# Kernel tuning notes

Measured on AMD Instinct MI355X. Metric: run time of the kernel, lower is better.

Reference implementation:

```python
import jax, jax.numpy as jnp
import numpy as np

B, C, IMG, P = 32, 3, 224, 16
D, H, L, F, NCLS = 768, 12, 12, 3072, 1000
NP = (IMG // P) ** 2  # 196
DH = D // H  # 64
EPS = 1e-5


def _ln(x, g, b):
    m = jnp.mean(x, axis=-1, keepdims=True)
    v = jnp.mean(jnp.square(x - m), axis=-1, keepdims=True)
    return (x - m) * jax.lax.rsqrt(v + EPS) * g + b


def setup_inputs() -> dict:
    key = jax.random.key(0)
    ks = iter(jax.random.split(key, 32))
    s = 0.02
    rn = lambda shape: jax.random.normal(next(ks), shape, dtype=jnp.float32) * s
    inp = {
        "x": jax.random.normal(next(ks), (B, C, IMG, IMG), dtype=jnp.float32),
        "Wp": rn((P * P * C, D)), "bp": jnp.zeros((D,), jnp.float32),
        "cls": rn((1, 1, D)), "pos": rn((1, NP + 1, D)),
        # per-layer stacked params (leading dim L)
        "ln1_g": jnp.ones((L, D), jnp.float32), "ln1_b": jnp.zeros((L, D), jnp.float32),
        "Wq": rn((L, H, D, DH)), "bq": jnp.zeros((L, H, DH), jnp.float32),
        "Wk": rn((L, H, D, DH)), "bk": jnp.zeros((L, H, DH), jnp.float32),
        "Wv": rn((L, H, D, DH)), "bv": jnp.zeros((L, H, DH), jnp.float32),
        "Wo": rn((L, D, D)), "bo": jnp.zeros((L, D), jnp.float32),
        "ln2_g": jnp.ones((L, D), jnp.float32), "ln2_b": jnp.zeros((L, D), jnp.float32),
        "W1": rn((L, D, F)), "b1": jnp.zeros((L, F), jnp.float32),
        "W2": rn((L, F, D)), "b2": jnp.zeros((L, D), jnp.float32),
        # classification head
        "hln_g": jnp.ones((D,), jnp.float32), "hln_b": jnp.zeros((D,), jnp.float32),
        "hW1": rn((D, D)), "hb1": jnp.zeros((D,), jnp.float32),
        "hW2": rn((D, NCLS)), "hb2": jnp.zeros((NCLS,), jnp.float32),
    }
    return inp


def _vit(x, Wp, bp, cls, pos, ln1_g, ln1_b, Wq, bq, Wk, bk, Wv, bv, Wo, bo,
         ln2_g, ln2_b, W1, b1, W2, b2, hln_g, hln_b, hW1, hb1, hW2, hb2):
    b = x.shape[0]
    g = IMG // P
    # nn.Unfold(k=16, s=16): channel order (c, kh, kw), patch order (ph, pw)
    patches = x.reshape(b, C, g, P, g, P).transpose(0, 2, 4, 1, 3, 5).reshape(b, NP, C * P * P)
    h = patches @ Wp + bp  # [b, NP, D]
    h = jnp.concatenate([jnp.broadcast_to(cls, (b, 1, D)), h], axis=1) + pos  # [b, S, D]

    scale = 1.0 / jnp.sqrt(jnp.asarray(DH, h.dtype))

    def step(h, p):
        g1, b1_, wq, bq_, wk, bk_, wv, bv_, wo, bo_, g2, b2_, w1, bb1, w2, bb2 = p
        xn = _ln(h, g1, b1_)
        q = jnp.einsum('bsd,hde->bhse', xn, wq) + bq_[:, None, :]
        k = jnp.einsum('bsd,hde->bhse', xn, wk) + bk_[:, None, :]
        v = jnp.einsum('bsd,hde->bhse', xn, wv) + bv_[:, None, :]
        scores = jnp.einsum('bhse,bhte->bhst', q, k) * scale
        attn = jax.nn.softmax(scores, axis=-1)
        o = jnp.einsum('bhst,bhte->bhse', attn, v)  # [b,H,S,DH]
        o = o.transpose(0, 2, 1, 3).reshape(b, -1, D)  # concat heads
        h = o @ wo + bo_ + h
        xn = _ln(h, g2, b2_)
        h = jax.nn.gelu(xn @ w1 + bb1, approximate=False) @ w2 + bb2 + h
        return h, None

    params = (ln1_g, ln1_b, Wq, bq, Wk, bk, Wv, bv, Wo, bo, ln2_g, ln2_b, W1, b1, W2, b2)
    h, _ = jax.lax.scan(step, h, params)

    c = h[:, 0, :]
    c = _ln(c, hln_g, hln_b)
    return jax.nn.gelu(c @ hW1 + hb1, approximate=False) @ hW2 + hb2


def reference(x, Wp, bp, cls, pos, ln1_g, ln1_b, Wq, bq, Wk, bk, Wv, bv, Wo, bo,
              ln2_g, ln2_b, W1, b1, W2, b2, hln_g, hln_b, hW1, hb1, hW2, hb2):
    return _vit(x, Wp, bp, cls, pos, ln1_g, ln1_b, Wq, bq, Wk, bk, Wv, bv, Wo, bo,
                ln2_g, ln2_b, W1, b1, W2, b2, hln_g, hln_b, hW1, hb1, hW2, hb2)
```

## Files before the change

### kernel.cpp

```cpp
#include <hip/hip_runtime.h>

typedef unsigned short u16;
typedef __attribute__((ext_vector_type(8))) short short8;
typedef __attribute__((ext_vector_type(4))) float f32x4;

#define NTOK 6304
#define SP 197

#define OFF_WQKVT 0L
#define OFF_WOT   42467328L
#define OFF_W1T   56623104L
#define OFF_W2T   113246208L
#define OFF_WPT   169869312L
#define OFF_BQKV  171048960L
#define OFF_H     171159552L
#define OFF_XN    190525440L
#define OFF_QKV   200208384L
#define OFF_SC    229257216L
#define OFF_PM1   288867840L
#define OFF_VT    327599616L
#define OFF_CN    340182528L
#define OFF_T1    340280832L
#define WS_NEEDED 340379136L

__device__ __forceinline__ u16 f2bf(float x) {
  unsigned int u = __float_as_uint(x);
  u += 0x7fffu + ((u >> 16) & 1u);
  return (u16)(u >> 16);
}

__device__ __forceinline__ float gelu_f(float x) {
  return 0.5f * x * (1.0f + erff(x * 0.70710678118654752f));
}

__device__ __forceinline__ void gload_lds16(const void* g, void* l) {
  __builtin_amdgcn_global_load_lds(
      (const __attribute__((address_space(1))) unsigned int*)g,
      (__attribute__((address_space(3))) unsigned int*)l, 16, 0, 0);
}

__device__ __forceinline__ void stage_tile(const u16* src, int ld,
                                           int row0, int maxrow, int k0,
                                           char* ldsbase, int t) {
  const int wbase = t & 192;
#pragma unroll
  for (int p = 0; p < 4; ++p) {
    int idx = p * 256 + t;
    int r = idx >> 3;
    int cl = idx & 7;
    int cg = cl ^ (r & 7);
    int rr = row0 + r;
    rr = rr > maxrow ? maxrow : rr;
    const u16* g = src + (long)rr * ld + (k0 + cg * 8);
    char* lp = ldsbase + (long)(p * 256 + wbase) * 16;
    gload_lds16(g, lp);
  }
}

template <bool BIAS, bool GELU, bool RES, bool OBF16, bool REMAP>
__global__ __launch_bounds__(256, 3) void gemm_k(
    const u16* __restrict__ A, int lda,
    const u16* __restrict__ Bm, int ldb,
    void* Cv, int ldc,
    const float* __restrict__ bias, const float* res, int ldres,
    int M, int N, int K, int tilesN) {
  __shared__ float4 smemv[2048];
  char* smem = (char*)smemv;

  const int t = threadIdx.x;
  const int nwg = gridDim.x;
  const int orig = blockIdx.x;
  const int q8 = nwg >> 3, r8 = nwg & 7;
  const int xcd = orig & 7, loc = orig >> 3;
  const int wg =
      (xcd < r8 ? xcd * (q8 + 1) : r8 * (q8 + 1) + (xcd - r8) * q8) + loc;
  const int tn = wg % tilesN, tm = wg / tilesN;
  const int m0 = tm * 128, n0 = tn * 128;
  const int l = t & 63;
  const int lr = l & 15, kb = l >> 4;
  const int wr = (t >> 7) & 1, wc = (t >> 6) & 1;

  const f32x4 zf = {0.f, 0.f, 0.f, 0.f};
  f32x4 acc[4][4];
#pragma unroll
  for (int m = 0; m < 4; ++m)
#pragma unroll
    for (int n = 0; n < 4; ++n) acc[m][n] = zf;

  const int KT = K >> 6;
  for (int kt = 0; kt < KT; ++kt) {
    stage_tile(A, lda, m0, M - 1, kt * 64, smem, t);
    stage_tile(Bm, ldb, n0, N - 1, kt * 64, smem + 16384, t);
    __syncthreads();
    const char* Ab = smem;
    const char* Bb = smem + 16384;
#pragma unroll
    for (int kk = 0; kk < 2; ++kk) {
      const int cla = ((kk << 2) + kb) ^ (lr & 7);
      short8 af[4], bfv[4];
#pragma unroll
      for (int m = 0; m < 4; ++m)
        af[m] = *(const short8*)(Ab + ((wr * 64 + m * 16 + lr) * 128 + cla * 16));
#pragma unroll
      for (int n = 0; n < 4; ++n)
        bfv[n] = *(const short8*)(Bb + ((wc * 64 + n * 16 + lr) * 128 + cla * 16));
#pragma unroll
      for (int m = 0; m < 4; ++m)
#pragma unroll
        for (int n = 0; n < 4; ++n)
          acc[m][n] = __builtin_amdgcn_mfma_f32_16x16x32_bf16(af[m], bfv[n],
                                                              acc[m][n], 0, 0, 0);
    }
    __syncthreads();
  }

#pragma unroll
  for (int n = 0; n < 4; ++n) {
    const int gc = n0 + wc * 64 + n * 16 + lr;
    if (gc >= N) continue;
    const float bv = BIAS ? bias[gc] : 0.0f;
#pragma unroll
    for (int m = 0; m < 4; ++m) {
#pragma unroll
      for (int j = 0; j < 4; ++j) {
        const int gr = m0 + wr * 64 + m * 16 + kb * 4 + j;
        if (gr >= M) continue;
        float v = acc[m][n][j] + bv;
        if (RES) v += res[(long)gr * ldres + gc];
        if (GELU) v = gelu_f(v);
        long orow = gr;
        if (REMAP) orow = (long)(gr / 196) * 197 + (gr % 196) + 1;
        if (OBF16)
          ((u16*)Cv)[orow * (long)ldc + gc] = f2bf(v);
        else
          ((float*)Cv)[orow * (long)ldc + gc] = v;
      }
    }
  }
}

__global__ __launch_bounds__(256) void k_attn(const u16* __restrict__ qkv,
                                              u16* __restrict__ o) {
  __shared__ __align__(16) u16 Kb[208 * 72];
  __shared__ __align__(16) u16 Vt[64 * 232];
  __shared__ __align__(16) u16 Pl[4][16 * 232];

  const int t = threadIdx.x;
  const int z = blockIdx.x;
  const int b = z / 12, hh = z % 12;
  const long qbase = (long)b * SP * 2304 + hh * 64;

#pragma unroll
  for (int p = 0; p < 7; ++p) {
    int idx = p * 256 + t;
    int row = idx >> 3, c = idx & 7;
    short8 kv = {0, 0, 0, 0, 0, 0, 0, 0};
    short8 vv = {0, 0, 0, 0, 0, 0, 0, 0};
    if (row < SP) {
      kv = *(const short8*)(qkv + qbase + 768 + (long)row * 2304 + c * 8);
      vv = *(const short8*)(qkv + qbase + 1536 + (long)row * 2304 + c * 8);
    }
    if (row < 208) *(short8*)(&Kb[row * 72 + c * 8]) = kv;
#pragma unroll
    for (int j = 0; j < 8; ++j) Vt[(c * 8 + j) * 232 + row] = ((const u16*)&vv)[j];
  }
  __syncthreads();

  const int l = t & 63, wid = t >> 6;
  const int lr = l & 15, kb = l >> 4;
  u16* Pw = Pl[wid];
  const f32x4 zf = {0.f, 0.f, 0.f, 0.f};

  for (int st = wid; st < 13; st += 4) {
    int qrow = st * 16 + lr;
    qrow = qrow > SP - 1 ? SP - 1 : qrow;
    short8 qf[2];
#pragma unroll
    for (int kk = 0; kk < 2; ++kk)
      qf[kk] = *(const short8*)(qkv + qbase + (long)qrow * 2304 + kk * 32 + kb * 8);

    f32x4 s[13];
#pragma unroll
    for (int nt = 0; nt < 13; ++nt) {
      s[nt] = zf;
#pragma unroll
      for (int kk = 0; kk < 2; ++kk) {
        short8 kf = *(const short8*)(&Kb[(nt * 16 + lr) * 72 + kk * 32 + kb * 8]);
        s[nt] = __builtin_amdgcn_mfma_f32_16x16x32_bf16(qf[kk], kf, s[nt], 0, 0, 0);
      }
    }

    float mx[4] = {-1e30f, -1e30f, -1e30f, -1e30f};
#pragma unroll
    for (int nt = 0; nt < 13; ++nt) {
      const bool pred = (nt < 12) | (lr < 5);
#pragma unroll
      for (int j = 0; j < 4; ++j) {
        float v = s[nt][j] * 0.125f;
        s[nt][j] = v;
        if (pred) mx[j] = fmaxf(mx[j], v);
      }
    }
#pragma unroll
    for (int o4 = 1; o4 < 16; o4 <<= 1)
#pragma unroll
      for (int j = 0; j < 4; ++j) mx[j] = fmaxf(mx[j], __shfl_xor(mx[j], o4));
    float sum[4] = {0.f, 0.f, 0.f, 0.f};
#pragma unroll
    for (int nt = 0; nt < 13; ++nt) {
      const bool pred = (nt < 12) | (lr < 5);
#pragma unroll
      for (int j = 0; j < 4; ++j) {
        float p = pred ? __expf(s[nt][j] - mx[j]) : 0.f;
        s[nt][j] = p;
        sum[j] += p;
      }
    }
#pragma unroll
    for (int o4 = 1; o4 < 16; o4 <<= 1)
#pragma unroll
      for (int j = 0; j < 4; ++j) sum[j] += __shfl_xor(sum[j], o4);
    float inv[4];
#pragma unroll
    for (int j = 0; j < 4; ++j) inv[j] = 1.0f / sum[j];

#pragma unroll
    for (int nt = 0; nt < 13; ++nt)
#pragma unroll
      for (int j = 0; j < 4; ++j)
        Pw[(kb * 4 + j) * 232 + nt * 16 + lr] = f2bf(s[nt][j] * inv[j]);
#pragma unroll
    for (int j = 0; j < 4; ++j) Pw[(kb * 4 + j) * 232 + 208 + lr] = 0;

    short8 pf[7];
#pragma unroll
    for (int kk = 0; kk < 7; ++kk)
      pf[kk] = *(const short8*)(&Pw[lr * 232 + kk * 32 + kb * 8]);
#pragma unroll
    for (int dt = 0; dt < 4; ++dt) {
      f32x4 oacc = zf;
#pragma unroll
      for (int kk = 0; kk < 7; ++kk) {
        short8 vf = *(const short8*)(&Vt[(dt * 16 + lr) * 232 + kk * 32 + kb * 8]);
        oacc = __builtin_amdgcn_mfma_f32_16x16x32_bf16(pf[kk], vf, oacc, 0, 0, 0);
      }
#pragma unroll
      for (int j = 0; j < 4; ++j) {
        int qr = st * 16 + kb * 4 + j;
        if (qr < SP)
          o[((long)b * SP + qr) * 768 + hh * 64 + dt * 16 + lr] = f2bf(oacc[j]);
      }
    }
  }
}

__global__ void k_wt64(const float* __restrict__ W, u16* __restrict__ out,
                       int sel) {
  __shared__ float tile[32][33];
  const int z = blockIdx.z;
  const int ly = z / 12, hh = z % 12;
  const float* ip = W + (long)z * 768 * 64;
  u16* op = out + (long)ly * 2304 * 768 + ((long)sel * 768 + hh * 64) * 768;
  const int c0 = blockIdx.x * 32, r0 = blockIdx.y * 32;
  const int tx = threadIdx.x, ty = threadIdx.y;
#pragma unroll
  for (int i = 0; i < 4; ++i)
    tile[ty + i * 8][tx] = ip[(long)(r0 + ty + i * 8) * 64 + c0 + tx];
  __syncthreads();
#pragma unroll
  for (int i = 0; i < 4; ++i)
    op[(long)(c0 + ty + i * 8) * 768 + r0 + tx] = f2bf(tile[tx][ty + i * 8]);
}

__global__ void k_bqkv(const float* __restrict__ bq, const float* __restrict__ bk,
                       const float* __restrict__ bv, float* __restrict__ out) {
  int idx = blockIdx.x * 256 + threadIdx.x;
  if (idx >= 27648) return;
  int c = idx % 2304, ly = idx / 2304;
  int sel = c / 768, cc = c % 768;
  const float* b = sel == 0 ? bq : (sel == 1 ? bk : bv);
  out[idx] = b[ly * 768 + cc];
}

__global__ void k_transpose(const float* __restrict__ in, u16* __restrict__ out,
                            int R, int C) {
  __shared__ float tile[32][33];
  long zoff = (long)blockIdx.z * R * C;
  const float* ip = in + zoff;
  u16* op = out + zoff;
  int c0 = blockIdx.x * 32, r0 = blockIdx.y * 32;
  int tx = threadIdx.x, ty = threadIdx.y;
#pragma unroll
  for (int i = 0; i < 4; ++i)
    tile[ty + i * 8][tx] = ip[(long)(r0 + ty + i * 8) * C + c0 + tx];
  __syncthreads();
#pragma unroll
  for (int i = 0; i < 4; ++i)
    op[(long)(c0 + ty + i * 8) * R + r0 + tx] = f2bf(tile[tx][ty + i * 8]);
}

__global__ void k_patchify(const float* __restrict__ x, u16* __restrict__ out) {
  long idx = (long)blockIdx.x * 256 + threadIdx.x;
  int f = (int)(idx % 768);
  long rp = idx / 768;
  int p = (int)(rp % 196), b = (int)(rp / 196);
  int gy = p / 14, gx = p % 14;
  int c = f >> 8, rem = f & 255;
  int i = rem >> 4, j = rem & 15;
  out[idx] = f2bf(x[(((long)b * 3 + c) * 224 + gy * 16 + i) * 224 + gx * 16 + j]);
}

__global__ void k_add_pos(float* h, const float* __restrict__ cls,
                          const float* __restrict__ pos) {
  long idx = (long)blockIdx.x * 256 + threadIdx.x;
  int d = (int)(idx % 768);
  long rs = idx / 768;
  int s = (int)(rs % 197);
  if (s == 0)
    h[idx] = cls[d] + pos[d];
  else
    h[idx] += pos[(long)s * 768 + d];
}

__global__ __launch_bounds__(256) void k_ln(const float* __restrict__ in,
                                            const float* __restrict__ g,
                                            const float* __restrict__ b,
                                            u16* __restrict__ out, int rows) {
  int w = threadIdx.x >> 6, l = threadIdx.x & 63;
  int row = blockIdx.x * 4 + w;
  if (row >= rows) return;
  const float4* ip = (const float4*)(in + (long)row * 768);
  float4 v[3];
  float s = 0.f, sq = 0.f;
#pragma unroll
  for (int i = 0; i < 3; ++i) {
    v[i] = ip[i * 64 + l];
    s += v[i].x + v[i].y + v[i].z + v[i].w;
    sq += v[i].x * v[i].x + v[i].y * v[i].y + v[i].z * v[i].z + v[i].w * v[i].w;
  }
#pragma unroll
  for (int o = 1; o < 64; o <<= 1) {
    s += __shfl_xor(s, o);
    sq += __shfl_xor(sq, o);
  }
  const float m = s * (1.f / 768.f);
  const float rs = rsqrtf(sq * (1.f / 768.f) - m * m + 1e-5f);
  ushort4* op = (ushort4*)(out + (long)row * 768);
#pragma unroll
  for (int i = 0; i < 3; ++i) {
    int c4 = (i * 64 + l) * 4;
    float4 gv = *(const float4*)(g + c4);
    float4 bv = *(const float4*)(b + c4);
    ushort4 o4;
    o4.x = f2bf((v[i].x - m) * rs * gv.x + bv.x);
    o4.y = f2bf((v[i].y - m) * rs * gv.y + bv.y);
    o4.z = f2bf((v[i].z - m) * rs * gv.z + bv.z);
    o4.w = f2bf((v[i].w - m) * rs * gv.w + bv.w);
    op[i * 64 + l] = o4;
  }
}

__global__ void k_head_ln(const float* __restrict__ h, const float* __restrict__ g,
                          const float* __restrict__ b, float* __restrict__ out) {
  const int bb = blockIdx.x, l = threadIdx.x;
  const float4* ip = (const float4*)(h + (long)bb * 197 * 768);
  float4 v[3];
  float s = 0.f, sq = 0.f;
#pragma unroll
  for (int i = 0; i < 3; ++i) {
    v[i] = ip[i * 64 + l];
    s += v[i].x + v[i].y + v[i].z + v[i].w;
    sq += v[i].x * v[i].x + v[i].y * v[i].y + v[i].z * v[i].z + v[i].w * v[i].w;
  }
#pragma unroll
  for (int o = 1; o < 64; o <<= 1) {
    s += __shfl_xor(s, o);
    sq += __shfl_xor(sq, o);
  }
  const float m = s * (1.f / 768.f);
  const float rs = rsqrtf(sq * (1.f / 768.f) - m * m + 1e-5f);
  float4* op = (float4*)(out + bb * 768);
#pragma unroll
  for (int i = 0; i < 3; ++i) {
    int c4 = (i * 64 + l) * 4;
    float4 gv = *(const float4*)(g + c4);
    float4 bv = *(const float4*)(b + c4);
    float4 o4;
    o4.x = (v[i].x - m) * rs * gv.x + bv.x;
    o4.y = (v[i].y - m) * rs * gv.y + bv.y;
    o4.z = (v[i].z - m) * rs * gv.z + bv.z;
    o4.w = (v[i].w - m) * rs * gv.w + bv.w;
    op[i * 64 + l] = o4;
  }
}

template <bool GELU>
__global__ __launch_bounds__(256) void k_head_gemm(
    const float* __restrict__ in, const float* __restrict__ W,
    const float* __restrict__ bias, float* __restrict__ out, int K, int N) {
  __shared__ float partial[4][64];
  const int b = blockIdx.y;
  const int cl = threadIdx.x & 63;
  const int c = blockIdx.x * 64 + cl;
  const int kp = threadIdx.x >> 6;
  const int kc = K >> 2;
  float s = 0.f;
  if (c < N) {
    const float* ip = in + (long)b * K + kp * kc;
    const float* wp = W + (long)(kp * kc) * N + c;
    for (int k = 0; k < kc; ++k) s = fmaf(ip[k], wp[(long)k * N], s);
  }
  partial[kp][cl] = s;
  __syncthreads();
  if (kp == 0 && c < N) {
    float v = partial[0][cl] + partial[1][cl] + partial[2][cl] + partial[3][cl] +
              bias[c];
    if (GELU) v = gelu_f(v);
    out[(long)b * N + c] = v;
  }
}

extern "C" void kernel_launch(void* const* d_in, const int* in_sizes, int n_in,
                              void* d_out, int out_size, void* d_ws, size_t ws_size,
                              hipStream_t stream) {
  (void)in_sizes; (void)n_in; (void)out_size;
  if ((long)ws_size < WS_NEEDED) return;

  const float* x = (const float*)d_in[0];
  const float* Wp = (const float*)d_in[1];
  const float* bp = (const float*)d_in[2];
  const float* cls = (const float*)d_in[3];
  const float* pos = (const float*)d_in[4];
  const float* ln1g = (const float*)d_in[5];
  const float* ln1b = (const float*)d_in[6];
  const float* Wq = (const float*)d_in[7];
  const float* bq = (const float*)d_in[8];
  const float* Wk = (const float*)d_in[9];
  const float* bk = (const float*)d_in[10];
  const float* Wv = (const float*)d_in[11];
  const float* bv = (const float*)d_in[12];
  const float* Wo = (const float*)d_in[13];
  const float* bo = (const float*)d_in[14];
  const float* ln2g = (const float*)d_in[15];
  const float* ln2b = (const float*)d_in[16];
  const float* W1 = (const float*)d_in[17];
  const float* b1 = (const float*)d_in[18];
  const float* W2 = (const float*)d_in[19];
  const float* b2 = (const float*)d_in[20];
  const float* hlng = (const float*)d_in[21];
  const float* hlnb = (const float*)d_in[22];
  const float* hW1 = (const float*)d_in[23];
  const float* hb1 = (const float*)d_in[24];
  const float* hW2 = (const float*)d_in[25];
  const float* hb2 = (const float*)d_in[26];

  char* ws = (char*)d_ws;
  u16* wqkvt = (u16*)(ws + OFF_WQKVT);
  u16* wot = (u16*)(ws + OFF_WOT);
  u16* w1t = (u16*)(ws + OFF_W1T);
  u16* w2t = (u16*)(ws + OFF_W2T);
  u16* wpt = (u16*)(ws + OFF_WPT);
  float* bqkv = (float*)(ws + OFF_BQKV);
  float* h = (float*)(ws + OFF_H);
  u16* xn = (u16*)(ws + OFF_XN);
  u16* qkv = (u16*)(ws + OFF_QKV);
  u16* pbuf = qkv;
  u16* m1 = (u16*)(ws + OFF_PM1);
  float* cn = (float*)(ws + OFF_CN);
  float* t1 = (float*)(ws + OFF_T1);

  k_wt64<<<dim3(2, 24, 144), dim3(32, 8), 0, stream>>>(Wq, wqkvt, 0);
  k_wt64<<<dim3(2, 24, 144), dim3(32, 8), 0, stream>>>(Wk, wqkvt, 1);
  k_wt64<<<dim3(2, 24, 144), dim3(32, 8), 0, stream>>>(Wv, wqkvt, 2);
  k_bqkv<<<108, 256, 0, stream>>>(bq, bk, bv, bqkv);
  k_transpose<<<dim3(24, 24, 12), dim3(32, 8), 0, stream>>>(Wo, wot, 768, 768);
  k_transpose<<<dim3(96, 24, 12), dim3(32, 8), 0, stream>>>(W1, w1t, 768, 3072);
  k_transpose<<<dim3(24, 96, 12), dim3(32, 8), 0, stream>>>(W2, w2t, 3072, 768);
  k_transpose<<<dim3(24, 24, 1), dim3(32, 8), 0, stream>>>(Wp, wpt, 768, 768);

  k_patchify<<<18816, 256, 0, stream>>>(x, pbuf);
  gemm_k<true, false, false, false, true><<<49 * 6, 256, 0, stream>>>(
      pbuf, 768, wpt, 768, h, 768, bp, nullptr, 0, 6272, 768, 768, 6);
  k_add_pos<<<18912, 256, 0, stream>>>(h, cls, pos);

  for (int ly = 0; ly < 12; ++ly) {
    k_ln<<<1576, 256, 0, stream>>>(h, ln1g + ly * 768, ln1b + ly * 768, xn, NTOK);
    gemm_k<true, false, false, true, false><<<50 * 18, 256, 0, stream>>>(
        xn, 768, wqkvt + (long)ly * 2304 * 768, 768, qkv, 2304,
        bqkv + ly * 2304, nullptr, 0, NTOK, 2304, 768, 18);
    k_attn<<<384, 256, 0, stream>>>(qkv, xn);
    gemm_k<true, false, true, false, false><<<50 * 6, 256, 0, stream>>>(
        xn, 768, wot + (long)ly * 768 * 768, 768, h, 768,
        bo + ly * 768, h, 768, NTOK, 768, 768, 6);
    k_ln<<<1576, 256, 0, stream>>>(h, ln2g + ly * 768, ln2b + ly * 768, xn, NTOK);
    gemm_k<true, true, false, true, false><<<50 * 24, 256, 0, stream>>>(
        xn, 768, w1t + (long)ly * 3072 * 768, 768, m1, 3072,
        b1 + ly * 3072, nullptr, 0, NTOK, 3072, 768, 24);
    gemm_k<true, false, true, false, false><<<50 * 6, 256, 0, stream>>>(
        m1, 3072, w2t + (long)ly * 768 * 3072, 3072, h, 768,
        b2 + ly * 768, h, 768, NTOK, 768, 3072, 6);
  }

  k_head_ln<<<32, 64, 0, stream>>>(h, hlng, hlnb, cn);
  k_head_gemm<true><<<dim3(12, 32), 256, 0, stream>>>(cn, hW1, hb1, t1, 768, 768);
  k_head_gemm<false><<<dim3(16, 32), 256, 0, stream>>>(t1, hW2, hb2, (float*)d_out,
                                                       768, 1000);
}
```

Measured before the change: 3.429 ms.

## Template GEMM tile sizes and double-buffer LDS staging with prefetch

Replaces the fixed 128x128 GEMM with a templated kernel that double-buffers the LDS tiles, issuing async global-to-LDS loads for the next K-step while the current step runs MFMAs, and drops one barrier per iteration. The QKV and FC1 GEMMs move to 256x256 tiles with 8 waves (512 threads) so each operand load is reused more. The cost is more LDS and registers per block and lower occupancy. The larger tiles also leave fewer blocks, which may underfill the CUs.

```diff
diff --git a/kernel.cpp b/kernel.cpp
--- a/kernel.cpp
+++ b/kernel.cpp
@@ -39,35 +39,29 @@
       (__attribute__((address_space(3))) unsigned int*)l, 16, 0, 0);
 }
 
-__device__ __forceinline__ void stage_tile(const u16* src, int ld,
-                                           int row0, int maxrow, int k0,
-                                           char* ldsbase, int t) {
-  const int wbase = t & 192;
-#pragma unroll
-  for (int p = 0; p < 4; ++p) {
-    int idx = p * 256 + t;
-    int r = idx >> 3;
-    int cl = idx & 7;
-    int cg = cl ^ (r & 7);
-    int rr = row0 + r;
-    rr = rr > maxrow ? maxrow : rr;
-    const u16* g = src + (long)rr * ld + (k0 + cg * 8);
-    char* lp = ldsbase + (long)(p * 256 + wbase) * 16;
-    gload_lds16(g, lp);
-  }
-}
-
-template <bool BIAS, bool GELU, bool RES, bool OBF16, bool REMAP>
-__global__ __launch_bounds__(256, 3) void gemm_k(
+template <int BM, int BN, int WM, int WN, bool BIAS, bool GELU, bool RES,
+          bool OBF16, bool REMAP>
+__global__ __launch_bounds__(WM * WN * 64, 2) void gemm2(
     const u16* __restrict__ A, int lda,
     const u16* __restrict__ Bm, int ldb,
     void* Cv, int ldc,
     const float* __restrict__ bias, const float* res, int ldres,
     int M, int N, int K, int tilesN) {
-  __shared__ float4 smemv[2048];
-  char* smem = (char*)smemv;
+  constexpr int THREADS = WM * WN * 64;
+  constexpr int TM = BM / WM, TN = BN / WN;
+  constexpr int FM = TM / 16, FN = TN / 16;
+  constexpr int APT = (BM * 8) / THREADS;
+  constexpr int BPT = (BN * 8) / THREADS;
+  constexpr int ABYTES = BM * 128;
+  constexpr int BUF = ABYTES + BN * 128;
+  __shared__ __align__(16) char smem[2 * BUF];
 
   const int t = threadIdx.x;
+  const int l = t & 63;
+  const int lr = l & 15, kb = (l >> 4) & 3;
+  const int wid = t >> 6;
+  const int wr = wid / WN, wc = wid % WN;
+
   const int nwg = gridDim.x;
   const int orig = blockIdx.x;
   const int q8 = nwg >> 3, r8 = nwg & 7;
@@ -75,57 +69,80 @@
   const int wg =
       (xcd < r8 ? xcd * (q8 + 1) : r8 * (q8 + 1) + (xcd - r8) * q8) + loc;
   const int tn = wg % tilesN, tm = wg / tilesN;
-  const int m0 = tm * 128, n0 = tn * 128;
-  const int l = t & 63;
-  const int lr = l & 15, kb = l >> 4;
-  const int wr = (t >> 7) & 1, wc = (t >> 6) & 1;
+  const int m0 = tm * BM, n0 = tn * BN;
+  const int Mm1 = M - 1, Nm1 = N - 1;
 
   const f32x4 zf = {0.f, 0.f, 0.f, 0.f};
-  f32x4 acc[4][4];
-#pragma unroll
-  for (int m = 0; m < 4; ++m)
-#pragma unroll
-    for (int n = 0; n < 4; ++n) acc[m][n] = zf;
-
-  const int KT = K >> 6;
-  for (int kt = 0; kt < KT; ++kt) {
-    stage_tile(A, lda, m0, M - 1, kt * 64, smem, t);
-    stage_tile(Bm, ldb, n0, N - 1, kt * 64, smem + 16384, t);
+  f32x4 acc[FM][FN];
+#pragma unroll
+  for (int fm = 0; fm < FM; ++fm)
+#pragma unroll
+    for (int fn = 0; fn < FN; ++fn) acc[fm][fn] = zf;
+
+  auto stage = [&](int kt, int d) {
+    const int k0 = kt << 6;
+    char* base = smem + d * BUF;
+#pragma unroll
+    for (int p = 0; p < APT; ++p) {
+      int idx = p * THREADS + t;
+      int r = idx >> 3, cl = idx & 7;
+      int rr = m0 + r;
+      rr = rr > Mm1 ? Mm1 : rr;
+      gload_lds16(A + (long)rr * lda + k0 + ((cl ^ (r & 7)) << 3),
+                  base + ((p * THREADS + (t & ~63)) << 4));
+    }
+    char* bbase = base + ABYTES;
+#pragma unroll
+    for (int p = 0; p < BPT; ++p) {
+      int idx = p * THREADS + t;
+      int r = idx >> 3, cl = idx & 7;
+      int rr = n0 + r;
+      rr = rr > Nm1 ? Nm1 : rr;
+      gload_lds16(Bm + (long)rr * ldb + k0 + ((cl ^ (r & 7)) << 3),
+                  bbase + ((p * THREADS + (t & ~63)) << 4));
+    }
+  };
+
+  const int nt = K >> 6;
+  stage(0, 0);
+  __syncthreads();
+
+  for (int kt = 0; kt < nt; ++kt) {
+    if (kt + 1 < nt) stage(kt + 1, (kt + 1) & 1);
+    const char* Ab = smem + (kt & 1) * BUF;
+    const char* Bb = Ab + ABYTES;
+#pragma unroll
+    for (int kk = 0; kk < 2; ++kk) {
+      const int ch = ((((kk << 2) | kb) ^ (lr & 7)) << 4);
+      short8 af[FM], bf[FN];
+#pragma unroll
+      for (int fm = 0; fm < FM; ++fm)
+        af[fm] = *(const short8*)(Ab + (wr * TM + fm * 16 + lr) * 128 + ch);
+#pragma unroll
+      for (int fn = 0; fn < FN; ++fn)
+        bf[fn] = *(const short8*)(Bb + (wc * TN + fn * 16 + lr) * 128 + ch);
+#pragma unroll
+      for (int fm = 0; fm < FM; ++fm)
+#pragma unroll
+        for (int fn = 0; fn < FN; ++fn)
+          acc[fm][fn] = __builtin_amdgcn_mfma_f32_16x16x32_bf16(af[fm], bf[fn],
+                                                                acc[fm][fn], 0, 0, 0);
+    }
     __syncthreads();
-    const char* Ab = smem;
-    const char* Bb = smem + 16384;
-#pragma unroll
-    for (int kk = 0; kk < 2; ++kk) {
-      const int cla = ((kk << 2) + kb) ^ (lr & 7);
-      short8 af[4], bfv[4];
-#pragma unroll
-      for (int m = 0; m < 4; ++m)
-        af[m] = *(const short8*)(Ab + ((wr * 64 + m * 16 + lr) * 128 + cla * 16));
-#pragma unroll
-      for (int n = 0; n < 4; ++n)
-        bfv[n] = *(const short8*)(Bb + ((wc * 64 + n * 16 + lr) * 128 + cla * 16));
-#pragma unroll
-      for (int m = 0; m < 4; ++m)
-#pragma unroll
-        for (int n = 0; n < 4; ++n)
-          acc[m][n] = __builtin_amdgcn_mfma_f32_16x16x32_bf16(af[m], bfv[n],
-                                                              acc[m][n], 0, 0, 0);
-    }
-    __syncthreads();
-  }
-
-#pragma unroll
-  for (int n = 0; n < 4; ++n) {
-    const int gc = n0 + wc * 64 + n * 16 + lr;
+  }
+
+#pragma unroll
+  for (int fn = 0; fn < FN; ++fn) {
+    const int gc = n0 + wc * TN + fn * 16 + lr;
     if (gc >= N) continue;
     const float bv = BIAS ? bias[gc] : 0.0f;
 #pragma unroll
-    for (int m = 0; m < 4; ++m) {
+    for (int fm = 0; fm < FM; ++fm) {
 #pragma unroll
       for (int j = 0; j < 4; ++j) {
-        const int gr = m0 + wr * 64 + m * 16 + kb * 4 + j;
+        const int gr = m0 + wr * TM + fm * 16 + kb * 4 + j;
         if (gr >= M) continue;
-        float v = acc[m][n][j] + bv;
+        float v = acc[fm][fn][j] + bv;
         if (RES) v += res[(long)gr * ldres + gc];
         if (GELU) v = gelu_f(v);
         long orow = gr;
@@ -479,24 +496,24 @@
   k_transpose<<<dim3(24, 24, 1), dim3(32, 8), 0, stream>>>(Wp, wpt, 768, 768);
 
   k_patchify<<<18816, 256, 0, stream>>>(x, pbuf);
-  gemm_k<true, false, false, false, true><<<49 * 6, 256, 0, stream>>>(
+  gemm2<128, 128, 2, 2, true, false, false, false, true><<<294, 256, 0, stream>>>(
       pbuf, 768, wpt, 768, h, 768, bp, nullptr, 0, 6272, 768, 768, 6);
   k_add_pos<<<18912, 256, 0, stream>>>(h, cls, pos);
 
   for (int ly = 0; ly < 12; ++ly) {
     k_ln<<<1576, 256, 0, stream>>>(h, ln1g + ly * 768, ln1b + ly * 768, xn, NTOK);
-    gemm_k<true, false, false, true, false><<<50 * 18, 256, 0, stream>>>(
+    gemm2<256, 256, 2, 4, true, false, false, true, false><<<225, 512, 0, stream>>>(
         xn, 768, wqkvt + (long)ly * 2304 * 768, 768, qkv, 2304,
-        bqkv + ly * 2304, nullptr, 0, NTOK, 2304, 768, 18);
+        bqkv + ly * 2304, nullptr, 0, NTOK, 2304, 768, 9);
     k_attn<<<384, 256, 0, stream>>>(qkv, xn);
-    gemm_k<true, false, true, false, false><<<50 * 6, 256, 0, stream>>>(
+    gemm2<128, 128, 2, 2, true, false, true, false, false><<<300, 256, 0, stream>>>(
         xn, 768, wot + (long)ly * 768 * 768, 768, h, 768,
         bo + ly * 768, h, 768, NTOK, 768, 768, 6);
     k_ln<<<1576, 256, 0, stream>>>(h, ln2g + ly * 768, ln2b + ly * 768, xn, NTOK);
-    gemm_k<true, true, false, true, false><<<50 * 24, 256, 0, stream>>>(
+    gemm2<256, 256, 2, 4, true, true, false, true, false><<<300, 512, 0, stream>>>(
         xn, 768, w1t + (long)ly * 3072 * 768, 768, m1, 3072,
-        b1 + ly * 3072, nullptr, 0, NTOK, 3072, 768, 24);
-    gemm_k<true, false, true, false, false><<<50 * 6, 256, 0, stream>>>(
+        b1 + ly * 3072, nullptr, 0, NTOK, 3072, 768, 12);
+    gemm2<128, 128, 2, 2, true, false, true, false, false><<<300, 256, 0, stream>>>(
         m1, 3072, w2t + (long)ly * 768 * 3072, 3072, h, 768,
         b2 + ly * 768, h, 768, NTOK, 768, 3072, 6);
   }
```

After: 4.302 ms. 1.25x slower.
